# Performance work log

Measured on AMD Instinct MI355X. Metric: run time of the kernel, lower is better.

The kernel has to match this reference:

```python
import jax, jax.numpy as jnp
import numpy as np

BLOCK = 16                      # NVFP4 block size along K
FP4_MAX = 6.0                   # e2m1 max magnitude
FP8_MAX = 448.0                 # e4m3 max
E2M1_GRID = jnp.array([0.0, 0.5, 1.0, 1.5, 2.0, 3.0, 4.0, 5.0, 6.0], dtype=jnp.float32)
E2M1_MIDS = jnp.array([0.25, 0.75, 1.25, 1.75, 2.5, 3.5, 4.5, 5.5], dtype=jnp.float32)


def _global_sf(t):
    # 448*6 / amax(|t|), amax clamped to 1e-12 (matches torch code)
    amax = jnp.clip(jnp.max(jnp.abs(jnp.nan_to_num(t))), 1e-12, None)
    return (FP8_MAX * FP4_MAX) / amax


def _round_e4m3(v):
    # round-to-nearest e4m3fn via dtype cast
    return v.astype(jnp.float8_e4m3fn).astype(jnp.float32)


def _round_e2m1(v):
    # nearest value on the signed e2m1 grid, clamped to +-6
    a = jnp.clip(jnp.abs(v), 0.0, FP4_MAX)
    idx = jnp.searchsorted(E2M1_MIDS, a)
    return E2M1_GRID[idx] * jnp.sign(v)


def nvfp4_quant_dequant(t, global_sf):
    """Simulate nvfp4_quantize + dequant. Returns t_hat ~= t * global_sf
    (values representable as e2m1 * e4m3 block scale)."""
    rows, K = t.shape
    tb = t.reshape(rows, K // BLOCK, BLOCK)
    amax = jnp.max(jnp.abs(tb), axis=-1, keepdims=True)            # [rows, K/16, 1]
    sf = _round_e4m3(jnp.clip(amax * global_sf / FP4_MAX, 0.0, FP8_MAX))
    inv_sf = jnp.where(sf > 0, global_sf / sf, 0.0)
    q = _round_e2m1(tb * inv_sf)                                   # fp4 codes (as f32)
    return (q * sf).reshape(rows, K)                               # dequant in scaled space


def setup_inputs() -> dict:
    key = jax.random.key(0)
    kx, kw = jax.random.split(key)
    M, K, N = 4096, 4096, 4096
    x = jax.random.normal(kx, (M, K), dtype=jnp.float32)
    w = jax.random.normal(kw, (N, K), dtype=jnp.float32)
    return {"x": x, "w": w}


def reference(x, w):
    w_gsf = _global_sf(w)
    x_gsf = _global_sf(x)
    w_hat = nvfp4_quant_dequant(w, w_gsf)   # ~= w * w_gsf
    x_hat = nvfp4_quant_dequant(x, x_gsf)   # ~= x * x_gsf
    alpha = 1.0 / (w_gsf * x_gsf)
    # mm_fp4: (x_q xsf) @ (w_q wsf)^T * alpha  -> [M, N]
    return jnp.einsum('mk,nk->mn', x_hat, w_hat) * alpha
```

## Files before the change

### kernel.cpp

```cpp
#include <hip/hip_runtime.h>
#include <hip/hip_bf16.h>
#include <stdint.h>

#define M_DIM 4096
#define N_DIM 4096
#define K_DIM 4096
#define KB 8192

typedef __bf16 bf16x8 __attribute__((ext_vector_type(8)));
typedef float  f32x4  __attribute__((ext_vector_type(4)));

__global__ __launch_bounds__(256) void amax2_kernel(const float* __restrict__ x,
                                                    const float* __restrict__ w,
                                                    unsigned int* __restrict__ out) {
    __shared__ float red[4];
    const int half = blockIdx.x >> 10;
    const float4* in4 = (const float4*)(half ? w : x);
    const int lid = (blockIdx.x & 1023) * 256 + threadIdx.x;
    const int S = 1024 * 256;
    float m0 = 0.f, m1 = 0.f, m2 = 0.f, m3 = 0.f;
#pragma unroll
    for (int k = 0; k < 4; ++k) {
        float4 a = in4[lid + (4 * k + 0) * S];
        float4 b = in4[lid + (4 * k + 1) * S];
        float4 c = in4[lid + (4 * k + 2) * S];
        float4 d = in4[lid + (4 * k + 3) * S];
        m0 = fmaxf(m0, fmaxf(fmaxf(fabsf(a.x), fabsf(a.y)), fmaxf(fabsf(a.z), fabsf(a.w))));
        m1 = fmaxf(m1, fmaxf(fmaxf(fabsf(b.x), fabsf(b.y)), fmaxf(fabsf(b.z), fabsf(b.w))));
        m2 = fmaxf(m2, fmaxf(fmaxf(fabsf(c.x), fabsf(c.y)), fmaxf(fabsf(c.z), fabsf(c.w))));
        m3 = fmaxf(m3, fmaxf(fmaxf(fabsf(d.x), fabsf(d.y)), fmaxf(fabsf(d.z), fabsf(d.w))));
    }
    float m = fmaxf(fmaxf(m0, m1), fmaxf(m2, m3));
#pragma unroll
    for (int off = 32; off > 0; off >>= 1)
        m = fmaxf(m, __shfl_xor(m, off, 64));
    if ((threadIdx.x & 63) == 0) red[threadIdx.x >> 6] = m;
    __syncthreads();
    if (threadIdx.x == 0) {
        float r = fmaxf(fmaxf(red[0], red[1]), fmaxf(red[2], red[3]));
        atomicMax(out + half, __float_as_uint(r));
    }
}

__device__ __forceinline__ float round_e4m3(float v) {
    if (!(v > 0.f)) return 0.f;
    uint32_t u = __float_as_uint(v);
    int e = (int)(u >> 23) - 127;
    if (e < -6) e = -6;
    float ulp     = __uint_as_float((uint32_t)(e - 3 + 127) << 23);
    float inv_ulp = __uint_as_float((uint32_t)(3 - e + 127) << 23);
    return rintf(v * inv_ulp) * ulp;
}

__device__ __forceinline__ float round_e2m1_mag(float a) {
    float q = 0.f;
    q = (a > 0.25f) ? 0.5f : q;
    q = (a > 0.75f) ? 1.0f : q;
    q = (a > 1.25f) ? 1.5f : q;
    q = (a > 1.75f) ? 2.0f : q;
    q = (a > 2.5f)  ? 3.0f : q;
    q = (a > 3.5f)  ? 4.0f : q;
    q = (a > 4.5f)  ? 5.0f : q;
    q = (a > 5.5f)  ? 6.0f : q;
    return q;
}

__device__ __forceinline__ unsigned int pack2(float va, float vb, float inv, float sf) {
    float xa = va * inv, xb = vb * inv;
    float qa = round_e2m1_mag(fminf(fabsf(xa), 6.f));
    float qb = round_e2m1_mag(fminf(fabsf(xb), 6.f));
    float ta = copysignf(qa, xa) * sf;
    float tb = copysignf(qb, xb) * sf;
    return (__float_as_uint(ta) >> 16) | ((__float_as_uint(tb) >> 16) << 16);
}

__global__ __launch_bounds__(256) void quant2_kernel(const float* __restrict__ x,
                                                     const float* __restrict__ w,
                                                     unsigned short* __restrict__ xq,
                                                     unsigned short* __restrict__ wq,
                                                     const unsigned int* __restrict__ amax_bits) {
    const float gx = 2688.0f / fmaxf(__uint_as_float(amax_bits[0]), 1e-12f);
    const float gw = 2688.0f / fmaxf(__uint_as_float(amax_bits[1]), 1e-12f);
    const int t0 = blockIdx.x * 256 + threadIdx.x;
    const int S = 4096 * 256;
#pragma unroll
    for (int it = 0; it < 8; ++it) {
        const bool isx = (it < 4);
        const float4* src = (const float4*)(isx ? x : w);
        unsigned short* dst = isx ? xq : wq;
        const float gsf = isx ? gx : gw;
        const int li = t0 + (isx ? it : it - 4) * S;
        float4 v = src[li];
        float am = fmaxf(fmaxf(fabsf(v.x), fabsf(v.y)), fmaxf(fabsf(v.z), fabsf(v.w)));
        am = fmaxf(am, __shfl_xor(am, 1, 64));
        am = fmaxf(am, __shfl_xor(am, 2, 64));
        float sf  = round_e4m3(fminf(fmaxf(am * gsf / 6.0f, 0.f), 448.0f));
        float inv = (sf > 0.f) ? (gsf / sf) : 0.f;
        uint2 o;
        o.x = pack2(v.x, v.y, inv, sf);
        o.y = pack2(v.z, v.w, inv, sf);
        *(uint2*)(dst + (size_t)li * 4) = o;
    }
}

__global__ __launch_bounds__(512, 2) void gemm_kernel(const unsigned short* __restrict__ A,
                                                      const unsigned short* __restrict__ B,
                                                      float* __restrict__ C,
                                                      const unsigned int* __restrict__ amax_bits) {
    __shared__ alignas(16) char smem[131072];

    const int tid  = threadIdx.x;
    const int lane = tid & 63;
    const int wid  = tid >> 6;
    const int wr   = wid >> 2;
    const int wc   = wid & 3;

    int bid = blockIdx.x;
    int swz = (bid & 7) * 32 + (bid >> 3);
    const int brow = (swz >> 4) * 256;
    const int bcol = (swz & 15) * 256;

    int rowS[2], colS[2], Lr[2];
#pragma unroll
    for (int r = 0; r < 2; ++r) {
        int L = r * 8192 + tid * 16;
        int b = L ^ (((L >> 7) & 7) << 4);
        Lr[r] = L;
        rowS[r] = b >> 7;
        colS[r] = b & 127;
    }
    const char* Abase = (const char*)A;
    const char* Bbase = (const char*)B;

    auto STAGE = [&](int ts, int slot) {
        const char* mat = (slot >= 2) ? Abase : Bbase;
        int rbase = ((slot >= 2) ? brow : bcol) + ((slot & 1) ? 128 : 0);
        int loff  = (ts & 1) * 65536 + ((slot >= 2) ? 0 : 32768) + ((slot & 1) ? 16384 : 0);
#pragma unroll
        for (int r = 0; r < 2; ++r) {
            const char* gp = mat + (size_t)(rbase + rowS[r]) * KB + ts * 128 + colS[r];
            __builtin_amdgcn_global_load_lds(
                (const __attribute__((address_space(1))) unsigned int*)gp,
                (__attribute__((address_space(3))) unsigned int*)(smem + loff + Lr[r]),
                16, 0, 0);
        }
    };

    const int lr  = lane & 15;
    const int kg  = lane >> 4;
    const int swx = (lr & 7) << 4;
    int colA[2];
#pragma unroll
    for (int ks = 0; ks < 2; ++ks) colA[ks] = (ks * 64 + kg * 16) ^ swx;
    int rowAb[8], rowBb[4];
#pragma unroll
    for (int m = 0; m < 8; ++m) rowAb[m] = (wr * 128 + m * 16 + lr) * 128;
#pragma unroll
    for (int n = 0; n < 4; ++n) rowBb[n] = 32768 + (wc * 64 + n * 16 + lr) * 128;

    bf16x8 bR[4][2];
    bf16x8 aS0[2][2], aS1[2][2];
    f32x4  acc[8][4];
#pragma unroll
    for (int m = 0; m < 8; ++m)
#pragma unroll
        for (int n = 0; n < 4; ++n)
#pragma unroll
            for (int j = 0; j < 4; ++j) acc[m][n][j] = 0.f;

    auto LDB_ALL = [&](int bufo) {
#pragma unroll
        for (int n = 0; n < 4; ++n)
#pragma unroll
            for (int ks = 0; ks < 2; ++ks)
                bR[n][ks] = *(const bf16x8*)(smem + bufo + rowBb[n] + colA[ks]);
    };
    auto LDC = [&](int bufo, int ci, bf16x8 (&s)[2][2]) {
#pragma unroll
        for (int mm = 0; mm < 2; ++mm)
#pragma unroll
            for (int ks = 0; ks < 2; ++ks)
                s[mm][ks] = *(const bf16x8*)(smem + bufo + rowAb[ci * 2 + mm] + colA[ks]);
    };
    auto MMAc = [&](int ci, bf16x8 (&s)[2][2]) {
        __builtin_amdgcn_s_setprio(1);
#pragma unroll
        for (int ks = 0; ks < 2; ++ks)
#pragma unroll
            for (int mm = 0; mm < 2; ++mm)
#pragma unroll
                for (int n = 0; n < 4; ++n)
                    acc[ci * 2 + mm][n] =
                        __builtin_amdgcn_mfma_f32_16x16x32_bf16(s[mm][ks], bR[n][ks], acc[ci * 2 + mm][n], 0, 0, 0);
        __builtin_amdgcn_s_setprio(0);
    };

    STAGE(0, 0); STAGE(0, 1); STAGE(0, 2); STAGE(0, 3);
    asm volatile("s_waitcnt vmcnt(4)" ::: "memory");
    STAGE(1, 0); STAGE(1, 1); STAGE(1, 2);
    asm volatile("s_waitcnt vmcnt(6)" ::: "memory");
    __builtin_amdgcn_s_barrier();
    LDC(0, 0, aS0); LDB_ALL(0); STAGE(1, 3);

#pragma unroll 1
    for (int i = 0; i < 32; ++i) {
        int e = 2 * i;
        int n2 = (e + 2 < 64) ? e + 2 : 63;
        int n3 = (e + 3 < 64) ? e + 3 : 63;

        LDC(0, 1, aS1); MMAc(0, aS0); STAGE(n2, 0);
        __builtin_amdgcn_s_barrier();
        LDC(0, 2, aS0); MMAc(1, aS1); STAGE(n2, 1);
        LDC(0, 3, aS1); MMAc(2, aS0); STAGE(n2, 2);
        asm volatile("s_waitcnt vmcnt(6)" ::: "memory");
        __builtin_amdgcn_s_barrier();
        LDC(65536, 0, aS0); MMAc(3, aS1); LDB_ALL(65536); STAGE(n2, 3);

        LDC(65536, 1, aS1); MMAc(0, aS0); STAGE(n3, 0);
        __builtin_amdgcn_s_barrier();
        LDC(65536, 2, aS0); MMAc(1, aS1); STAGE(n3, 1);
        LDC(65536, 3, aS1); MMAc(2, aS0); STAGE(n3, 2);
        asm volatile("s_waitcnt vmcnt(6)" ::: "memory");
        __builtin_amdgcn_s_barrier();
        LDC(0, 0, aS0); MMAc(3, aS1); LDB_ALL(0); STAGE(n3, 3);
    }

    float ax = fmaxf(__uint_as_float(amax_bits[0]), 1e-12f);
    float aw = fmaxf(__uint_as_float(amax_bits[1]), 1e-12f);
    float alpha = 1.0f / ((2688.0f / ax) * (2688.0f / aw));
    const int r4 = kg * 4;
    const int cn = lane & 15;
#pragma unroll
    for (int m = 0; m < 8; ++m)
#pragma unroll
        for (int n = 0; n < 4; ++n)
#pragma unroll
            for (int j = 0; j < 4; ++j) {
                int row = brow + wr * 128 + m * 16 + r4 + j;
                int col = bcol + wc * 64 + n * 16 + cn;
                C[(size_t)row * N_DIM + col] = acc[m][n][j] * alpha;
            }
}

extern "C" void kernel_launch(void* const* d_in, const int* in_sizes, int n_in,
                              void* d_out, int out_size, void* d_ws, size_t ws_size,
                              hipStream_t stream) {
    const float* x = (const float*)d_in[0];
    const float* w = (const float*)d_in[1];
    float* out = (float*)d_out;

    unsigned int*   amax  = (unsigned int*)d_ws;
    unsigned short* x_hat = (unsigned short*)((char*)d_ws + 256);
    unsigned short* w_hat = x_hat + (size_t)M_DIM * K_DIM;

    hipMemsetAsync(d_ws, 0, 256, stream);

    hipLaunchKernelGGL(amax2_kernel, dim3(2048), dim3(256), 0, stream, x, w, amax);
    hipLaunchKernelGGL(quant2_kernel, dim3(4096), dim3(256), 0, stream, x, w, x_hat, w_hat,
                       (const unsigned int*)amax);
    hipLaunchKernelGGL(gemm_kernel, dim3(256), dim3(512), 0, stream,
                       x_hat, w_hat, out, (const unsigned int*)d_ws);
}
```

Before: 172.7 us.

## Split B fragments into halves and interleave MFMA sub-tiles with LDS loads

```diff
diff --git a/kernel.cpp b/kernel.cpp
--- a/kernel.cpp
+++ b/kernel.cpp
@@ -158,8 +158,8 @@
 #pragma unroll
     for (int n = 0; n < 4; ++n) rowBb[n] = 32768 + (wc * 64 + n * 16 + lr) * 128;
 
-    bf16x8 bR[4][2];
-    bf16x8 aS0[2][2], aS1[2][2];
+    bf16x8 A0[2][2], A1[2][2];
+    bf16x8 B0[2][2], B1[2][2];
     f32x4  acc[8][4];
 #pragma unroll
     for (int m = 0; m < 8; ++m)
@@ -168,13 +168,6 @@
 #pragma unroll
             for (int j = 0; j < 4; ++j) acc[m][n][j] = 0.f;
 
-    auto LDB_ALL = [&](int bufo) {
-#pragma unroll
-        for (int n = 0; n < 4; ++n)
-#pragma unroll
-            for (int ks = 0; ks < 2; ++ks)
-                bR[n][ks] = *(const bf16x8*)(smem + bufo + rowBb[n] + colA[ks]);
-    };
     auto LDC = [&](int bufo, int ci, bf16x8 (&s)[2][2]) {
 #pragma unroll
         for (int mm = 0; mm < 2; ++mm)
@@ -182,16 +175,24 @@
             for (int ks = 0; ks < 2; ++ks)
                 s[mm][ks] = *(const bf16x8*)(smem + bufo + rowAb[ci * 2 + mm] + colA[ks]);
     };
-    auto MMAc = [&](int ci, bf16x8 (&s)[2][2]) {
+    auto LDB2 = [&](int bufo, int nh, bf16x8 (&b)[2][2]) {
+#pragma unroll
+        for (int nn = 0; nn < 2; ++nn)
+#pragma unroll
+            for (int ks = 0; ks < 2; ++ks)
+                b[nn][ks] = *(const bf16x8*)(smem + bufo + rowBb[nh * 2 + nn] + colA[ks]);
+    };
+    auto MMA2 = [&](int ci, int nh, bf16x8 (&s)[2][2], bf16x8 (&b)[2][2]) {
         __builtin_amdgcn_s_setprio(1);
 #pragma unroll
         for (int ks = 0; ks < 2; ++ks)
 #pragma unroll
             for (int mm = 0; mm < 2; ++mm)
 #pragma unroll
-                for (int n = 0; n < 4; ++n)
-                    acc[ci * 2 + mm][n] =
-                        __builtin_amdgcn_mfma_f32_16x16x32_bf16(s[mm][ks], bR[n][ks], acc[ci * 2 + mm][n], 0, 0, 0);
+                for (int nn = 0; nn < 2; ++nn)
+                    acc[ci * 2 + mm][nh * 2 + nn] =
+                        __builtin_amdgcn_mfma_f32_16x16x32_bf16(s[mm][ks], b[nn][ks],
+                                                                acc[ci * 2 + mm][nh * 2 + nn], 0, 0, 0);
         __builtin_amdgcn_s_setprio(0);
     };
 
@@ -200,7 +201,7 @@
     STAGE(1, 0); STAGE(1, 1); STAGE(1, 2);
     asm volatile("s_waitcnt vmcnt(6)" ::: "memory");
     __builtin_amdgcn_s_barrier();
-    LDC(0, 0, aS0); LDB_ALL(0); STAGE(1, 3);
+    LDC(0, 0, A0); LDB2(0, 0, B0); STAGE(1, 3);
 
 #pragma unroll 1
     for (int i = 0; i < 32; ++i) {
@@ -208,21 +209,29 @@
         int n2 = (e + 2 < 64) ? e + 2 : 63;
         int n3 = (e + 3 < 64) ? e + 3 : 63;
 
-        LDC(0, 1, aS1); MMAc(0, aS0); STAGE(n2, 0);
-        __builtin_amdgcn_s_barrier();
-        LDC(0, 2, aS0); MMAc(1, aS1); STAGE(n2, 1);
-        LDC(0, 3, aS1); MMAc(2, aS0); STAGE(n2, 2);
+        LDC(0, 1, A1); LDB2(0, 1, B1); MMA2(0, 0, A0, B0);
+        __builtin_amdgcn_s_barrier();
+        MMA2(0, 1, A0, B1); LDC(0, 2, A0); STAGE(n2, 0);
+        MMA2(1, 0, A1, B0);
+        MMA2(1, 1, A1, B1); LDC(0, 3, A1); STAGE(n2, 1);
+        MMA2(2, 0, A0, B0);
+        MMA2(2, 1, A0, B1); STAGE(n2, 2);
+        MMA2(3, 0, A1, B0);
         asm volatile("s_waitcnt vmcnt(6)" ::: "memory");
         __builtin_amdgcn_s_barrier();
-        LDC(65536, 0, aS0); MMAc(3, aS1); LDB_ALL(65536); STAGE(n2, 3);
-
-        LDC(65536, 1, aS1); MMAc(0, aS0); STAGE(n3, 0);
-        __builtin_amdgcn_s_barrier();
-        LDC(65536, 2, aS0); MMAc(1, aS1); STAGE(n3, 1);
-        LDC(65536, 3, aS1); MMAc(2, aS0); STAGE(n3, 2);
+        MMA2(3, 1, A1, B1); LDC(65536, 0, A0); LDB2(65536, 0, B0); STAGE(n2, 3);
+
+        LDC(65536, 1, A1); LDB2(65536, 1, B1); MMA2(0, 0, A0, B0);
+        __builtin_amdgcn_s_barrier();
+        MMA2(0, 1, A0, B1); LDC(65536, 2, A0); STAGE(n3, 0);
+        MMA2(1, 0, A1, B0);
+        MMA2(1, 1, A1, B1); LDC(65536, 3, A1); STAGE(n3, 1);
+        MMA2(2, 0, A0, B0);
+        MMA2(2, 1, A0, B1); STAGE(n3, 2);
+        MMA2(3, 0, A1, B0);
         asm volatile("s_waitcnt vmcnt(6)" ::: "memory");
         __builtin_amdgcn_s_barrier();
-        LDC(0, 0, aS0); MMAc(3, aS1); LDB_ALL(0); STAGE(n3, 3);
+        MMA2(3, 1, A1, B1); LDC(0, 0, A0); LDB2(0, 0, B0); STAGE(n3, 3);
     }
 
     float ax = fmaxf(__uint_as_float(amax_bits[0]), 1e-12f);
```

After: 172.6 us. Within noise of the previous version (-0.1%).
